# Kernel tuning notes

Hardware: AMD Instinct MI355X
Metric: run time of the kernel (lower is better)

## Reference

```python
import jax, jax.numpy as jnp
import numpy as np

B, F, D = 16384, 256, 128
H = [512, 256]
OUT = 8
VOCAB = 100000


def setup_inputs() -> dict:
    key = jax.random.key(0)
    ks = jax.random.split(key, 16)
    s = lambda k, *sh: jax.random.normal(k, sh, jnp.float32) * 0.05
    return dict(
        features=jax.random.normal(ks[0], (B, F), jnp.float32),
        ent_idx=jax.random.randint(ks[1], (B,), 0, VOCAB),
        target=jax.random.randint(ks[2], (B,), 0, OUT),
        Wf=s(ks[3], F, D), bf=jnp.zeros((D,), jnp.float32),
        Wu=s(ks[4], D, D), bu=jnp.zeros((D,), jnp.float32),
        w_cf=s(ks[5], D), w_fc=s(ks[6], D),
        w_ef=s(ks[7], D), w_fe=s(ks[8], D),
        b_c=jnp.zeros((1,), jnp.float32), b_e=jnp.zeros((1,), jnp.float32),
        head_tab=s(ks[9], VOCAB, D), ent_tab=s(ks[10], VOCAB, D),
        W0=s(ks[11], 2 * D, H[0]), b0=jnp.zeros((H[0],), jnp.float32),
        W1=s(ks[12], H[0], H[1]), b1=jnp.zeros((H[1],), jnp.float32),
        W2=s(ks[13], H[1], OUT), b2=jnp.zeros((OUT,), jnp.float32),
    )


def cross_compress(f, e, w_cf, w_fc, w_ef, w_fe, b_c, b_e):
    # torch code builds c = f (outer) e of shape (B,D,D) then matmuls a (D,1)
    # vector; algebraically (f e^T) w = f * (e . w), so we use the O(B*D) form.
    ew_cf = e @ w_cf  # (B,)
    fw_fc = f @ w_fc
    ew_ef = e @ w_ef
    fw_fe = f @ w_fe
    new_f = f * ew_cf[:, None] + e * fw_fc[:, None] + b_c
    new_e = f * ew_ef[:, None] + e * fw_fe[:, None] + b_e
    return new_f, new_e


def reference(features, ent_idx, target, Wf, bf, Wu, bu, w_cf, w_fc, w_ef,
              w_fe, b_c, b_e, head_tab, ent_tab, W0, b0, W1, b1, W2, b2):
    # 'rec' branch of CompanyOperationEvaluation.forward (eval mode, dropout=id)
    cf = jax.nn.relu(features @ Wf + bf)          # feature_layer
    e = ent_tab[ent_idx]                           # entity_embed lookup
    h = head_tab[ent_idx]                          # head_embed lookup (same ids)
    for _ in range(2):
        cf = jax.nn.relu(cf @ Wu + bu)             # user_low_mlp_layer
        h, e = cross_compress(h, e, w_cf, w_fc, w_ef, w_fe, b_c, b_e)
    high = jnp.concatenate([cf, e], axis=1)        # (B, 2D)
    x = jax.nn.relu(high @ W0 + b0)
    x = jax.nn.relu(x @ W1 + b1)
    x = jax.nn.relu(x @ W2 + b2)                   # pred_last_layer
    prob = jax.nn.softmax(x, axis=1)
    return (prob, target)
```

## Files before the change

kernel.cpp:

```cpp
#include <hip/hip_runtime.h>
#include <hip/hip_bf16.h>


typedef __bf16 bf16x8 __attribute__((ext_vector_type(8)));
typedef float floatx4 __attribute__((ext_vector_type(4)));

__device__ __forceinline__ unsigned short f2bf(float x) {
  unsigned int u = __builtin_bit_cast(unsigned int, x);
  u = (u + 0x7FFFu + ((u >> 16) & 1u)) >> 16;
  return (unsigned short)u;
}
__device__ __forceinline__ float bf2f(unsigned short h) {
  return __builtin_bit_cast(float, (unsigned int)h << 16);
}

__global__ __launch_bounds__(256) void prep_kernel(
    const float* __restrict__ features, const int* __restrict__ ent_idx,
    const float* __restrict__ head_tab, const float* __restrict__ ent_tab,
    const float* __restrict__ Wf, const float* __restrict__ Wu,
    const float* __restrict__ W0, const float* __restrict__ W1,
    const float* __restrict__ W2,
    unsigned short* __restrict__ feat_bf, unsigned short* __restrict__ e_buf,
    unsigned short* __restrict__ h_buf,
    unsigned short* __restrict__ wfT, unsigned short* __restrict__ wuT,
    unsigned short* __restrict__ w0T, unsigned short* __restrict__ w1T,
    unsigned short* __restrict__ w2T) {
  const int bid = blockIdx.x, tid = threadIdx.x;
  if (bid < 2048) {
    size_t base = (size_t)bid * 2048 + (size_t)tid * 8;
    float4 f0 = *(const float4*)(features + base);
    float4 f1 = *(const float4*)(features + base + 4);
    uint4 v;
    v.x = (unsigned)f2bf(f0.x) | ((unsigned)f2bf(f0.y) << 16);
    v.y = (unsigned)f2bf(f0.z) | ((unsigned)f2bf(f0.w) << 16);
    v.z = (unsigned)f2bf(f1.x) | ((unsigned)f2bf(f1.y) << 16);
    v.w = (unsigned)f2bf(f1.z) | ((unsigned)f2bf(f1.w) << 16);
    *(uint4*)(feat_bf + base) = v;
  } else if (bid < 4096) {
    int r = (bid - 2048) * 8 + (tid >> 5);
    int c = (tid & 31) * 4;
    int idx = ent_idx[r];
    float4 ev = *(const float4*)(ent_tab + (size_t)idx * 128 + c);
    float4 hv = *(const float4*)(head_tab + (size_t)idx * 128 + c);
    uint2 eo, ho;
    eo.x = (unsigned)f2bf(ev.x) | ((unsigned)f2bf(ev.y) << 16);
    eo.y = (unsigned)f2bf(ev.z) | ((unsigned)f2bf(ev.w) << 16);
    ho.x = (unsigned)f2bf(hv.x) | ((unsigned)f2bf(hv.y) << 16);
    ho.y = (unsigned)f2bf(hv.z) | ((unsigned)f2bf(hv.w) << 16);
    *(uint2*)(e_buf + (size_t)r * 128 + c) = eo;
    *(uint2*)(h_buf + (size_t)r * 128 + c) = ho;
  } else {
    int g = (bid - 4096) * 256 + tid;
    if (g < 32768) {
      int k = g >> 7, n = g & 127;  wfT[n * 256 + k] = f2bf(Wf[g]);
    } else if (g < 49152) {
      int l = g - 32768; int k = l >> 7, n = l & 127;
      wuT[n * 128 + k] = f2bf(Wu[l]);
    } else if (g < 180224) {
      int l = g - 49152; int k = l >> 9, n = l & 511;
      w0T[n * 256 + k] = f2bf(W0[l]);
    } else if (g < 311296) {
      int l = g - 180224; int k = l >> 8, n = l & 255;
      w1T[n * 512 + k] = f2bf(W1[l]);
    } else {
      int l = g - 311296; int k = l >> 3, n = l & 7;
      w2T[n * 256 + k] = f2bf(W2[l]);
    }
  }
}

__global__ __launch_bounds__(256) void gemm_kernel(
    const unsigned short* __restrict__ A, const unsigned short* __restrict__ BT,
    const float* __restrict__ bias, unsigned short* __restrict__ C,
    int K, int ldc) {
  __shared__ __align__(16) unsigned short a_sh[128 * 72];
  __shared__ __align__(16) unsigned short b_sh[64 * 72];
  const int tid = threadIdx.x;
  const int bn = blockIdx.x, bm = blockIdx.y;
  const int lane = tid & 63;
  const int wave = tid >> 6;
  const int wm = wave & 1, wn = wave >> 1;
  const int m16 = lane & 15, quad = lane >> 4;

  floatx4 acc[4][2];
#pragma unroll
  for (int i = 0; i < 4; ++i)
#pragma unroll
    for (int j = 0; j < 2; ++j) acc[i][j] = (floatx4){0.f, 0.f, 0.f, 0.f};

  for (int k0 = 0; k0 < K; k0 += 64) {
#pragma unroll
    for (int i = 0; i < 4; ++i) {
      int chunk = i * 256 + tid;
      int row = chunk >> 3, seg = chunk & 7;
      *(uint4*)&a_sh[row * 72 + seg * 8] =
          *(const uint4*)(A + (size_t)(bm * 128 + row) * K + k0 + seg * 8);
    }
#pragma unroll
    for (int i = 0; i < 2; ++i) {
      int chunk = i * 256 + tid;
      int row = chunk >> 3, seg = chunk & 7;
      *(uint4*)&b_sh[row * 72 + seg * 8] =
          *(const uint4*)(BT + (size_t)(bn * 64 + row) * K + k0 + seg * 8);
    }
    __syncthreads();
#pragma unroll
    for (int kk = 0; kk < 64; kk += 32) {
      bf16x8 af[4], bfr[2];
#pragma unroll
      for (int mi = 0; mi < 4; ++mi)
        af[mi] = *(const bf16x8*)&a_sh[(wm * 64 + mi * 16 + m16) * 72 + kk + quad * 8];
#pragma unroll
      for (int ni = 0; ni < 2; ++ni)
        bfr[ni] = *(const bf16x8*)&b_sh[(wn * 32 + ni * 16 + m16) * 72 + kk + quad * 8];
#pragma unroll
      for (int mi = 0; mi < 4; ++mi)
#pragma unroll
        for (int ni = 0; ni < 2; ++ni)
          acc[mi][ni] = __builtin_amdgcn_mfma_f32_16x16x32_bf16(
              af[mi], bfr[ni], acc[mi][ni], 0, 0, 0);
    }
    __syncthreads();
  }
#pragma unroll
  for (int mi = 0; mi < 4; ++mi) {
#pragma unroll
    for (int ni = 0; ni < 2; ++ni) {
      int col = bn * 64 + wn * 32 + ni * 16 + m16;
      float bv = bias[col];
#pragma unroll
      for (int r = 0; r < 4; ++r) {
        int row = bm * 128 + wm * 64 + mi * 16 + quad * 4 + r;
        float v = acc[mi][ni][r] + bv;
        v = fmaxf(v, 0.f);
        C[(size_t)row * ldc + col] = f2bf(v);
      }
    }
  }
}

__global__ __launch_bounds__(64) void cross_kernel(
    const unsigned short* __restrict__ h_buf, const unsigned short* __restrict__ e_buf,
    const float* __restrict__ w_cf, const float* __restrict__ w_fc,
    const float* __restrict__ w_ef, const float* __restrict__ w_fe,
    const float* __restrict__ b_c, const float* __restrict__ b_e,
    unsigned short* __restrict__ high) {
  const int lane = threadIdx.x;
  const int rl = lane >> 4, seg = lane & 15;
  const int row = blockIdx.x * 4 + rl;
  const int cb = seg * 8;
  float h[8], e[8], wcf[8], wfc[8], wef[8], wfe[8];
  const unsigned short* hp = h_buf + (size_t)row * 128 + cb;
  const unsigned short* ep = e_buf + (size_t)row * 128 + cb;
#pragma unroll
  for (int j = 0; j < 8; ++j) { h[j] = bf2f(hp[j]); e[j] = bf2f(ep[j]); }
#pragma unroll
  for (int j = 0; j < 8; ++j) {
    wcf[j] = w_cf[cb + j]; wfc[j] = w_fc[cb + j];
    wef[j] = w_ef[cb + j]; wfe[j] = w_fe[cb + j];
  }
  const float bc = b_c[0], be = b_e[0];
#pragma unroll
  for (int it = 0; it < 2; ++it) {
    float d0 = 0, d1 = 0, d2 = 0, d3 = 0;
#pragma unroll
    for (int j = 0; j < 8; ++j) {
      d0 += e[j] * wcf[j];
      d1 += h[j] * wfc[j];
      d2 += e[j] * wef[j];
      d3 += h[j] * wfe[j];
    }
#pragma unroll
    for (int s = 1; s < 16; s <<= 1) {
      d0 += __shfl_xor(d0, s); d1 += __shfl_xor(d1, s);
      d2 += __shfl_xor(d2, s); d3 += __shfl_xor(d3, s);
    }
    float nh[8], ne[8];
#pragma unroll
    for (int j = 0; j < 8; ++j) {
      nh[j] = h[j] * d0 + e[j] * d1 + bc;
      ne[j] = h[j] * d2 + e[j] * d3 + be;
    }
#pragma unroll
    for (int j = 0; j < 8; ++j) { h[j] = nh[j]; e[j] = ne[j]; }
  }
  uint4 v;
  v.x = (unsigned)f2bf(e[0]) | ((unsigned)f2bf(e[1]) << 16);
  v.y = (unsigned)f2bf(e[2]) | ((unsigned)f2bf(e[3]) << 16);
  v.z = (unsigned)f2bf(e[4]) | ((unsigned)f2bf(e[5]) << 16);
  v.w = (unsigned)f2bf(e[6]) | ((unsigned)f2bf(e[7]) << 16);
  *(uint4*)(high + (size_t)row * 256 + 128 + cb) = v;
}

__global__ __launch_bounds__(256) void final_kernel(
    const unsigned short* __restrict__ x1, const unsigned short* __restrict__ w2T,
    const float* __restrict__ b2, const int* __restrict__ target,
    float* __restrict__ out) {
  const int lane = threadIdx.x & 63;
  const int row = blockIdx.x * 4 + (threadIdx.x >> 6);
  float x[4];
  {
    const unsigned short* xp = x1 + (size_t)row * 256 + lane * 4;
#pragma unroll
    for (int j = 0; j < 4; ++j) x[j] = bf2f(xp[j]);
  }
  float p[8];
#pragma unroll
  for (int n = 0; n < 8; ++n) {
    const unsigned short* wp = w2T + n * 256 + lane * 4;
    float s = 0.f;
#pragma unroll
    for (int j = 0; j < 4; ++j) s += x[j] * bf2f(wp[j]);
    p[n] = s;
  }
#pragma unroll
  for (int s = 1; s < 64; s <<= 1) {
#pragma unroll
    for (int n = 0; n < 8; ++n) p[n] += __shfl_xor(p[n], s);
  }
  float mx = -1e30f;
#pragma unroll
  for (int n = 0; n < 8; ++n) {
    p[n] = fmaxf(p[n] + b2[n], 0.f);
    mx = fmaxf(mx, p[n]);
  }
  float sum = 0.f;
#pragma unroll
  for (int n = 0; n < 8; ++n) { p[n] = __expf(p[n] - mx); sum += p[n]; }
  const float inv = 1.f / sum;
  if (lane < 8) out[(size_t)row * 8 + lane] = p[lane] * inv;
  if (lane == 8) out[(size_t)(16384 * 8) + row] = (float)target[row];
}

extern "C" void kernel_launch(void* const* d_in, const int* in_sizes, int n_in,
                              void* d_out, int out_size, void* d_ws, size_t ws_size,
                              hipStream_t stream) {
  const float* features = (const float*)d_in[0];
  const int* ent_idx    = (const int*)d_in[1];
  const int* target     = (const int*)d_in[2];
  const float* Wf  = (const float*)d_in[3];
  const float* bf  = (const float*)d_in[4];
  const float* Wu  = (const float*)d_in[5];
  const float* bu  = (const float*)d_in[6];
  const float* w_cf = (const float*)d_in[7];
  const float* w_fc = (const float*)d_in[8];
  const float* w_ef = (const float*)d_in[9];
  const float* w_fe = (const float*)d_in[10];
  const float* b_c  = (const float*)d_in[11];
  const float* b_e  = (const float*)d_in[12];
  const float* head_tab = (const float*)d_in[13];
  const float* ent_tab  = (const float*)d_in[14];
  const float* W0 = (const float*)d_in[15];
  const float* b0 = (const float*)d_in[16];
  const float* W1 = (const float*)d_in[17];
  const float* b1 = (const float*)d_in[18];
  const float* W2 = (const float*)d_in[19];
  const float* b2 = (const float*)d_in[20];
  float* out = (float*)d_out;

  unsigned short* ws = (unsigned short*)d_ws;
  size_t off = 0;
  auto alloc = [&](size_t n) { unsigned short* p = ws + off; off += n; return p; };
  unsigned short* feat_bf = alloc(16384ull * 256);
  unsigned short* e_buf   = alloc(16384ull * 128);
  unsigned short* h_buf   = alloc(16384ull * 128);
  unsigned short* cf_a    = alloc(16384ull * 128);
  unsigned short* cf_b    = alloc(16384ull * 128);
  unsigned short* high    = alloc(16384ull * 256);
  unsigned short* x0      = alloc(16384ull * 512);
  unsigned short* x1      = alloc(16384ull * 256);
  unsigned short* wfT = alloc(32768);
  unsigned short* wuT = alloc(16384);
  unsigned short* w0T = alloc(131072);
  unsigned short* w1T = alloc(131072);
  unsigned short* w2T = alloc(2048);
  (void)ws_size; (void)in_sizes; (void)n_in; (void)out_size;

  prep_kernel<<<5320, 256, 0, stream>>>(features, ent_idx, head_tab, ent_tab,
      Wf, Wu, W0, W1, W2, feat_bf, e_buf, h_buf, wfT, wuT, w0T, w1T, w2T);
  gemm_kernel<<<dim3(2, 128), 256, 0, stream>>>(feat_bf, wfT, bf, cf_a, 256, 128);
  gemm_kernel<<<dim3(2, 128), 256, 0, stream>>>(cf_a, wuT, bu, cf_b, 128, 128);
  gemm_kernel<<<dim3(2, 128), 256, 0, stream>>>(cf_b, wuT, bu, high, 128, 256);
  cross_kernel<<<4096, 64, 0, stream>>>(h_buf, e_buf, w_cf, w_fc, w_ef, w_fe,
                                        b_c, b_e, high);
  gemm_kernel<<<dim3(8, 128), 256, 0, stream>>>(high, w0T, b0, x0, 256, 512);
  gemm_kernel<<<dim3(4, 128), 256, 0, stream>>>(x0, w1T, b1, x1, 512, 256);
  final_kernel<<<4096, 256, 0, stream>>>(x1, w2T, b2, target, out);
}
```

Before: 219.9 us.

## Fuse cross-compress into gather, chain cf MLP layers, fuse W1 GEMM with head

Folds the cross-compress computation into the embedding-gather prep stage, so h/e no longer round-trip through global memory. The feature cast and the three cf-MLP GEMMs become one kernel that keeps intermediates in LDS. The W1 GEMM is merged with the final W2 projection and softmax. Weight transposes now go through an LDS tile for coalesced writes. Together this cuts eight launches to four and removes several intermediate buffers, but the fused GEMMs read B operands straight from global memory with small 32-row tiles, which may reduce MFMA efficiency.

```diff
diff --git a/kernel.cpp b/kernel.cpp
--- a/kernel.cpp
+++ b/kernel.cpp
@@ -15,56 +15,166 @@
 }
 
 __global__ __launch_bounds__(256) void prep_kernel(
-    const float* __restrict__ features, const int* __restrict__ ent_idx,
-    const float* __restrict__ head_tab, const float* __restrict__ ent_tab,
+    const int* __restrict__ ent_idx, const float* __restrict__ head_tab,
+    const float* __restrict__ ent_tab,
+    const float* __restrict__ w_cf, const float* __restrict__ w_fc,
+    const float* __restrict__ w_ef, const float* __restrict__ w_fe,
+    const float* __restrict__ b_c, const float* __restrict__ b_e,
     const float* __restrict__ Wf, const float* __restrict__ Wu,
     const float* __restrict__ W0, const float* __restrict__ W1,
     const float* __restrict__ W2,
-    unsigned short* __restrict__ feat_bf, unsigned short* __restrict__ e_buf,
-    unsigned short* __restrict__ h_buf,
+    unsigned short* __restrict__ high,
     unsigned short* __restrict__ wfT, unsigned short* __restrict__ wuT,
     unsigned short* __restrict__ w0T, unsigned short* __restrict__ w1T,
     unsigned short* __restrict__ w2T) {
+  __shared__ unsigned short tile[32][34];
   const int bid = blockIdx.x, tid = threadIdx.x;
   if (bid < 2048) {
-    size_t base = (size_t)bid * 2048 + (size_t)tid * 8;
-    float4 f0 = *(const float4*)(features + base);
-    float4 f1 = *(const float4*)(features + base + 4);
-    uint4 v;
-    v.x = (unsigned)f2bf(f0.x) | ((unsigned)f2bf(f0.y) << 16);
-    v.y = (unsigned)f2bf(f0.z) | ((unsigned)f2bf(f0.w) << 16);
-    v.z = (unsigned)f2bf(f1.x) | ((unsigned)f2bf(f1.y) << 16);
-    v.w = (unsigned)f2bf(f1.z) | ((unsigned)f2bf(f1.w) << 16);
-    *(uint4*)(feat_bf + base) = v;
-  } else if (bid < 4096) {
-    int r = (bid - 2048) * 8 + (tid >> 5);
-    int c = (tid & 31) * 4;
-    int idx = ent_idx[r];
+    const int row = bid * 8 + (tid >> 5);
+    const int c = (tid & 31) * 4;
+    const int idx = ent_idx[row];
+    float4 hv = *(const float4*)(head_tab + (size_t)idx * 128 + c);
     float4 ev = *(const float4*)(ent_tab + (size_t)idx * 128 + c);
-    float4 hv = *(const float4*)(head_tab + (size_t)idx * 128 + c);
-    uint2 eo, ho;
-    eo.x = (unsigned)f2bf(ev.x) | ((unsigned)f2bf(ev.y) << 16);
-    eo.y = (unsigned)f2bf(ev.z) | ((unsigned)f2bf(ev.w) << 16);
-    ho.x = (unsigned)f2bf(hv.x) | ((unsigned)f2bf(hv.y) << 16);
-    ho.y = (unsigned)f2bf(hv.z) | ((unsigned)f2bf(hv.w) << 16);
-    *(uint2*)(e_buf + (size_t)r * 128 + c) = eo;
-    *(uint2*)(h_buf + (size_t)r * 128 + c) = ho;
+    float h[4] = {hv.x, hv.y, hv.z, hv.w};
+    float e[4] = {ev.x, ev.y, ev.z, ev.w};
+    float wcf[4], wfc[4], wef[4], wfe[4];
+#pragma unroll
+    for (int j = 0; j < 4; ++j) {
+      wcf[j] = w_cf[c + j]; wfc[j] = w_fc[c + j];
+      wef[j] = w_ef[c + j]; wfe[j] = w_fe[c + j];
+    }
+    const float bc = b_c[0], be = b_e[0];
+#pragma unroll
+    for (int it = 0; it < 2; ++it) {
+      float d0 = 0, d1 = 0, d2 = 0, d3 = 0;
+#pragma unroll
+      for (int j = 0; j < 4; ++j) {
+        d0 += e[j] * wcf[j]; d1 += h[j] * wfc[j];
+        d2 += e[j] * wef[j]; d3 += h[j] * wfe[j];
+      }
+#pragma unroll
+      for (int s = 1; s < 32; s <<= 1) {
+        d0 += __shfl_xor(d0, s); d1 += __shfl_xor(d1, s);
+        d2 += __shfl_xor(d2, s); d3 += __shfl_xor(d3, s);
+      }
+      float nh[4], ne[4];
+#pragma unroll
+      for (int j = 0; j < 4; ++j) {
+        nh[j] = h[j] * d0 + e[j] * d1 + bc;
+        ne[j] = h[j] * d2 + e[j] * d3 + be;
+      }
+#pragma unroll
+      for (int j = 0; j < 4; ++j) { h[j] = nh[j]; e[j] = ne[j]; }
+    }
+    uint2 v;
+    v.x = (unsigned)f2bf(e[0]) | ((unsigned)f2bf(e[1]) << 16);
+    v.y = (unsigned)f2bf(e[2]) | ((unsigned)f2bf(e[3]) << 16);
+    *(uint2*)(high + (size_t)row * 256 + 128 + c) = v;
+  } else if (bid < 2352) {
+    int t = bid - 2048;
+    const float* src; unsigned short* dst; int N, K, kt, nt;
+    if (t < 32)       { src = Wf; dst = wfT; N = 128; K = 256; kt = t >> 2;       nt = t & 3; }
+    else if (t < 48)  { t -= 32;  src = Wu; dst = wuT; N = 128; K = 128; kt = t >> 2; nt = t & 3; }
+    else if (t < 176) { t -= 48;  src = W0; dst = w0T; N = 512; K = 256; kt = t >> 4; nt = t & 15; }
+    else              { t -= 176; src = W1; dst = w1T; N = 256; K = 512; kt = t >> 3; nt = t & 7; }
+    {
+      int r = tid >> 3, cg = (tid & 7) * 4;
+      float4 v = *(const float4*)(src + (size_t)(kt * 32 + r) * N + nt * 32 + cg);
+      tile[r][cg + 0] = f2bf(v.x); tile[r][cg + 1] = f2bf(v.y);
+      tile[r][cg + 2] = f2bf(v.z); tile[r][cg + 3] = f2bf(v.w);
+    }
+    __syncthreads();
+    {
+      int rp = tid >> 3, cg = (tid & 7) * 4;
+      uint2 o;
+      o.x = (unsigned)tile[cg + 0][rp] | ((unsigned)tile[cg + 1][rp] << 16);
+      o.y = (unsigned)tile[cg + 2][rp] | ((unsigned)tile[cg + 3][rp] << 16);
+      *(uint2*)(dst + (size_t)(nt * 32 + rp) * K + kt * 32 + cg) = o;
+    }
   } else {
-    int g = (bid - 4096) * 256 + tid;
-    if (g < 32768) {
-      int k = g >> 7, n = g & 127;  wfT[n * 256 + k] = f2bf(Wf[g]);
-    } else if (g < 49152) {
-      int l = g - 32768; int k = l >> 7, n = l & 127;
-      wuT[n * 128 + k] = f2bf(Wu[l]);
-    } else if (g < 180224) {
-      int l = g - 49152; int k = l >> 9, n = l & 511;
-      w0T[n * 256 + k] = f2bf(W0[l]);
-    } else if (g < 311296) {
-      int l = g - 180224; int k = l >> 8, n = l & 255;
-      w1T[n * 512 + k] = f2bf(W1[l]);
-    } else {
-      int l = g - 311296; int k = l >> 3, n = l & 7;
-      w2T[n * 256 + k] = f2bf(W2[l]);
+#pragma unroll
+    for (int i = 0; i < 8; ++i) {
+      int g = tid * 8 + i, k = g >> 3, n = g & 7;
+      w2T[n * 256 + k] = f2bf(W2[g]);
+    }
+  }
+}
+
+template <int K, int LDA>
+__device__ __forceinline__ void mfma_layer(const unsigned short* A_sh,
+                                           const unsigned short* __restrict__ BT,
+                                           int rw, int nc, floatx4 acc[4]) {
+  const int lane = threadIdx.x & 63;
+  const int m16 = lane & 15, quad = lane >> 4;
+#pragma unroll
+  for (int nt = 0; nt < 4; ++nt) acc[nt] = (floatx4){0.f, 0.f, 0.f, 0.f};
+#pragma unroll
+  for (int kk = 0; kk < K; kk += 32) {
+    bf16x8 a = *(const bf16x8*)&A_sh[(rw + m16) * LDA + kk + quad * 8];
+#pragma unroll
+    for (int nt = 0; nt < 4; ++nt) {
+      bf16x8 b = *(const bf16x8*)(BT + (size_t)(nc + nt * 16 + m16) * K + kk + quad * 8);
+      acc[nt] = __builtin_amdgcn_mfma_f32_16x16x32_bf16(a, b, acc[nt], 0, 0, 0);
+    }
+  }
+}
+
+__device__ __forceinline__ void epi_lds(const floatx4 acc[4],
+                                        const float* __restrict__ bias, int rw,
+                                        int nc, unsigned short* buf, int ldb) {
+  const int lane = threadIdx.x & 63;
+  const int m16 = lane & 15, quad = lane >> 4;
+#pragma unroll
+  for (int nt = 0; nt < 4; ++nt) {
+    int col = nc + nt * 16 + m16;
+    float bv = bias[col];
+#pragma unroll
+    for (int r = 0; r < 4; ++r)
+      buf[(rw + quad * 4 + r) * ldb + col] = f2bf(fmaxf(acc[nt][r] + bv, 0.f));
+  }
+}
+
+__global__ __launch_bounds__(256) void cf_chain_kernel(
+    const float* __restrict__ features, const unsigned short* __restrict__ wfT,
+    const unsigned short* __restrict__ wuT, const float* __restrict__ bf_,
+    const float* __restrict__ bu, unsigned short* __restrict__ high) {
+  __shared__ __align__(16) unsigned short feat_sh[32 * 264];
+  __shared__ __align__(16) unsigned short buf0[32 * 136];
+  __shared__ __align__(16) unsigned short buf1[32 * 136];
+  const int tid = threadIdx.x;
+  const int r0 = blockIdx.x * 32;
+  {
+    int row = tid >> 3, c0 = (tid & 7) * 4;
+#pragma unroll
+    for (int i = 0; i < 8; ++i) {
+      int c = c0 + i * 32;
+      float4 v = *(const float4*)(features + (size_t)(r0 + row) * 256 + c);
+      uint2 o;
+      o.x = (unsigned)f2bf(v.x) | ((unsigned)f2bf(v.y) << 16);
+      o.y = (unsigned)f2bf(v.z) | ((unsigned)f2bf(v.w) << 16);
+      *(uint2*)&feat_sh[row * 264 + c] = o;
+    }
+  }
+  __syncthreads();
+  const int wave = tid >> 6;
+  const int rw = (wave >> 1) * 16, nc = (wave & 1) * 64;
+  floatx4 acc[4];
+  mfma_layer<256, 264>(feat_sh, wfT, rw, nc, acc);
+  epi_lds(acc, bf_, rw, nc, buf0, 136);
+  __syncthreads();
+  mfma_layer<128, 136>(buf0, wuT, rw, nc, acc);
+  epi_lds(acc, bu, rw, nc, buf1, 136);
+  __syncthreads();
+  mfma_layer<128, 136>(buf1, wuT, rw, nc, acc);
+  const int lane = tid & 63, m16 = lane & 15, quad = lane >> 4;
+#pragma unroll
+  for (int nt = 0; nt < 4; ++nt) {
+    int col = nc + nt * 16 + m16;
+    float bv = bu[col];
+#pragma unroll
+    for (int r = 0; r < 4; ++r) {
+      int row = r0 + rw + quad * 4 + r;
+      high[(size_t)row * 256 + col] = f2bf(fmaxf(acc[nt][r] + bv, 0.f));
     }
   }
 }
@@ -131,105 +241,96 @@
 #pragma unroll
       for (int r = 0; r < 4; ++r) {
         int row = bm * 128 + wm * 64 + mi * 16 + quad * 4 + r;
-        float v = acc[mi][ni][r] + bv;
-        v = fmaxf(v, 0.f);
+        float v = fmaxf(acc[mi][ni][r] + bv, 0.f);
         C[(size_t)row * ldc + col] = f2bf(v);
       }
     }
   }
 }
 
-__global__ __launch_bounds__(64) void cross_kernel(
-    const unsigned short* __restrict__ h_buf, const unsigned short* __restrict__ e_buf,
-    const float* __restrict__ w_cf, const float* __restrict__ w_fc,
-    const float* __restrict__ w_ef, const float* __restrict__ w_fe,
-    const float* __restrict__ b_c, const float* __restrict__ b_e,
-    unsigned short* __restrict__ high) {
-  const int lane = threadIdx.x;
-  const int rl = lane >> 4, seg = lane & 15;
-  const int row = blockIdx.x * 4 + rl;
-  const int cb = seg * 8;
-  float h[8], e[8], wcf[8], wfc[8], wef[8], wfe[8];
-  const unsigned short* hp = h_buf + (size_t)row * 128 + cb;
-  const unsigned short* ep = e_buf + (size_t)row * 128 + cb;
-#pragma unroll
-  for (int j = 0; j < 8; ++j) { h[j] = bf2f(hp[j]); e[j] = bf2f(ep[j]); }
-#pragma unroll
-  for (int j = 0; j < 8; ++j) {
-    wcf[j] = w_cf[cb + j]; wfc[j] = w_fc[cb + j];
-    wef[j] = w_ef[cb + j]; wfe[j] = w_fe[cb + j];
-  }
-  const float bc = b_c[0], be = b_e[0];
-#pragma unroll
-  for (int it = 0; it < 2; ++it) {
-    float d0 = 0, d1 = 0, d2 = 0, d3 = 0;
-#pragma unroll
-    for (int j = 0; j < 8; ++j) {
-      d0 += e[j] * wcf[j];
-      d1 += h[j] * wfc[j];
-      d2 += e[j] * wef[j];
-      d3 += h[j] * wfe[j];
-    }
-#pragma unroll
-    for (int s = 1; s < 16; s <<= 1) {
-      d0 += __shfl_xor(d0, s); d1 += __shfl_xor(d1, s);
-      d2 += __shfl_xor(d2, s); d3 += __shfl_xor(d3, s);
-    }
-    float nh[8], ne[8];
-#pragma unroll
-    for (int j = 0; j < 8; ++j) {
-      nh[j] = h[j] * d0 + e[j] * d1 + bc;
-      ne[j] = h[j] * d2 + e[j] * d3 + be;
-    }
-#pragma unroll
-    for (int j = 0; j < 8; ++j) { h[j] = nh[j]; e[j] = ne[j]; }
-  }
-  uint4 v;
-  v.x = (unsigned)f2bf(e[0]) | ((unsigned)f2bf(e[1]) << 16);
-  v.y = (unsigned)f2bf(e[2]) | ((unsigned)f2bf(e[3]) << 16);
-  v.z = (unsigned)f2bf(e[4]) | ((unsigned)f2bf(e[5]) << 16);
-  v.w = (unsigned)f2bf(e[6]) | ((unsigned)f2bf(e[7]) << 16);
-  *(uint4*)(high + (size_t)row * 256 + 128 + cb) = v;
-}
-
-__global__ __launch_bounds__(256) void final_kernel(
-    const unsigned short* __restrict__ x1, const unsigned short* __restrict__ w2T,
+__global__ __launch_bounds__(256) void gemm_w1_final_kernel(
+    const unsigned short* __restrict__ x0, const unsigned short* __restrict__ w1T,
+    const float* __restrict__ b1, const unsigned short* __restrict__ w2T,
     const float* __restrict__ b2, const int* __restrict__ target,
     float* __restrict__ out) {
-  const int lane = threadIdx.x & 63;
-  const int row = blockIdx.x * 4 + (threadIdx.x >> 6);
-  float x[4];
+  __shared__ __align__(16) unsigned short a_sh[32 * 72];
+  __shared__ __align__(16) unsigned short x1_sh[32 * 264];
+  __shared__ __align__(16) unsigned short w2_sh[2048];
+  const int tid = threadIdx.x;
+  const int r0 = blockIdx.x * 32;
+  *(uint4*)&w2_sh[tid * 8] = *(const uint4*)(w2T + tid * 8);
+  const int lane = tid & 63, wave = tid >> 6;
+  const int m16 = lane & 15, quad = lane >> 4;
+  const int rw = (wave >> 1) * 16, nc = (wave & 1) * 128;
+  floatx4 acc[8];
+#pragma unroll
+  for (int nt = 0; nt < 8; ++nt) acc[nt] = (floatx4){0.f, 0.f, 0.f, 0.f};
+  for (int k0 = 0; k0 < 512; k0 += 64) {
+    __syncthreads();
+    {
+      int row = tid >> 3, seg = tid & 7;
+      *(uint4*)&a_sh[row * 72 + seg * 8] =
+          *(const uint4*)(x0 + (size_t)(r0 + row) * 512 + k0 + seg * 8);
+    }
+    __syncthreads();
+#pragma unroll
+    for (int kk = 0; kk < 64; kk += 32) {
+      bf16x8 a = *(const bf16x8*)&a_sh[(rw + m16) * 72 + kk + quad * 8];
+#pragma unroll
+      for (int nt = 0; nt < 8; ++nt) {
+        bf16x8 b = *(const bf16x8*)(w1T + (size_t)(nc + nt * 16 + m16) * 512 +
+                                    k0 + kk + quad * 8);
+        acc[nt] = __builtin_amdgcn_mfma_f32_16x16x32_bf16(a, b, acc[nt], 0, 0, 0);
+      }
+    }
+  }
+#pragma unroll
+  for (int nt = 0; nt < 8; ++nt) {
+    int col = nc + nt * 16 + m16;
+    float bv = b1[col];
+#pragma unroll
+    for (int r = 0; r < 4; ++r)
+      x1_sh[(rw + quad * 4 + r) * 264 + col] = f2bf(fmaxf(acc[nt][r] + bv, 0.f));
+  }
+  __syncthreads();
   {
-    const unsigned short* xp = x1 + (size_t)row * 256 + lane * 4;
-#pragma unroll
-    for (int j = 0; j < 4; ++j) x[j] = bf2f(xp[j]);
-  }
-  float p[8];
-#pragma unroll
-  for (int n = 0; n < 8; ++n) {
-    const unsigned short* wp = w2T + n * 256 + lane * 4;
-    float s = 0.f;
-#pragma unroll
-    for (int j = 0; j < 4; ++j) s += x[j] * bf2f(wp[j]);
-    p[n] = s;
-  }
-#pragma unroll
-  for (int s = 1; s < 64; s <<= 1) {
-#pragma unroll
-    for (int n = 0; n < 8; ++n) p[n] += __shfl_xor(p[n], s);
-  }
-  float mx = -1e30f;
-#pragma unroll
-  for (int n = 0; n < 8; ++n) {
-    p[n] = fmaxf(p[n] + b2[n], 0.f);
-    mx = fmaxf(mx, p[n]);
-  }
-  float sum = 0.f;
-#pragma unroll
-  for (int n = 0; n < 8; ++n) { p[n] = __expf(p[n] - mx); sum += p[n]; }
-  const float inv = 1.f / sum;
-  if (lane < 8) out[(size_t)row * 8 + lane] = p[lane] * inv;
-  if (lane == 8) out[(size_t)(16384 * 8) + row] = (float)target[row];
+    int row = tid >> 3, q = tid & 7;
+    float p[8];
+#pragma unroll
+    for (int n = 0; n < 8; ++n) p[n] = 0.f;
+#pragma unroll
+    for (int jb = 0; jb < 4; ++jb) {
+      bf16x8 xv = *(const bf16x8*)&x1_sh[row * 264 + q * 32 + jb * 8];
+#pragma unroll
+      for (int n = 0; n < 8; ++n) {
+        bf16x8 wv = *(const bf16x8*)&w2_sh[n * 256 + q * 32 + jb * 8];
+#pragma unroll
+        for (int j = 0; j < 8; ++j) p[n] += (float)xv[j] * (float)wv[j];
+      }
+    }
+#pragma unroll
+    for (int s = 1; s < 8; s <<= 1)
+#pragma unroll
+      for (int n = 0; n < 8; ++n) p[n] += __shfl_xor(p[n], s);
+    if (q == 0) {
+      float mx = -1e30f;
+#pragma unroll
+      for (int n = 0; n < 8; ++n) {
+        p[n] = fmaxf(p[n] + b2[n], 0.f);
+        mx = fmaxf(mx, p[n]);
+      }
+      float sum = 0.f;
+#pragma unroll
+      for (int n = 0; n < 8; ++n) { p[n] = __expf(p[n] - mx); sum += p[n]; }
+      const float inv = 1.f / sum;
+      const int gr = r0 + row;
+      float4 o0 = {p[0] * inv, p[1] * inv, p[2] * inv, p[3] * inv};
+      float4 o1 = {p[4] * inv, p[5] * inv, p[6] * inv, p[7] * inv};
+      *(float4*)(out + (size_t)gr * 8) = o0;
+      *(float4*)(out + (size_t)gr * 8 + 4) = o1;
+      out[16384 * 8 + gr] = (float)target[gr];
+    }
+  }
 }
 
 extern "C" void kernel_launch(void* const* d_in, const int* in_sizes, int n_in,
@@ -239,7 +340,7 @@
   const int* ent_idx    = (const int*)d_in[1];
   const int* target     = (const int*)d_in[2];
   const float* Wf  = (const float*)d_in[3];
-  const float* bf  = (const float*)d_in[4];
+  const float* bf_ = (const float*)d_in[4];
   const float* Wu  = (const float*)d_in[5];
   const float* bu  = (const float*)d_in[6];
   const float* w_cf = (const float*)d_in[7];
@@ -261,29 +362,19 @@
   unsigned short* ws = (unsigned short*)d_ws;
   size_t off = 0;
   auto alloc = [&](size_t n) { unsigned short* p = ws + off; off += n; return p; };
-  unsigned short* feat_bf = alloc(16384ull * 256);
-  unsigned short* e_buf   = alloc(16384ull * 128);
-  unsigned short* h_buf   = alloc(16384ull * 128);
-  unsigned short* cf_a    = alloc(16384ull * 128);
-  unsigned short* cf_b    = alloc(16384ull * 128);
-  unsigned short* high    = alloc(16384ull * 256);
-  unsigned short* x0      = alloc(16384ull * 512);
-  unsigned short* x1      = alloc(16384ull * 256);
-  unsigned short* wfT = alloc(32768);
-  unsigned short* wuT = alloc(16384);
-  unsigned short* w0T = alloc(131072);
-  unsigned short* w1T = alloc(131072);
-  unsigned short* w2T = alloc(2048);
+  unsigned short* high = alloc(16384ull * 256);
+  unsigned short* x0   = alloc(16384ull * 512);
+  unsigned short* wfT  = alloc(32768);
+  unsigned short* wuT  = alloc(16384);
+  unsigned short* w0T  = alloc(131072);
+  unsigned short* w1T  = alloc(131072);
+  unsigned short* w2T  = alloc(2048);
   (void)ws_size; (void)in_sizes; (void)n_in; (void)out_size;
 
-  prep_kernel<<<5320, 256, 0, stream>>>(features, ent_idx, head_tab, ent_tab,
-      Wf, Wu, W0, W1, W2, feat_bf, e_buf, h_buf, wfT, wuT, w0T, w1T, w2T);
-  gemm_kernel<<<dim3(2, 128), 256, 0, stream>>>(feat_bf, wfT, bf, cf_a, 256, 128);
-  gemm_kernel<<<dim3(2, 128), 256, 0, stream>>>(cf_a, wuT, bu, cf_b, 128, 128);
-  gemm_kernel<<<dim3(2, 128), 256, 0, stream>>>(cf_b, wuT, bu, high, 128, 256);
-  cross_kernel<<<4096, 64, 0, stream>>>(h_buf, e_buf, w_cf, w_fc, w_ef, w_fe,
-                                        b_c, b_e, high);
+  prep_kernel<<<2353, 256, 0, stream>>>(ent_idx, head_tab, ent_tab,
+      w_cf, w_fc, w_ef, w_fe, b_c, b_e, Wf, Wu, W0, W1, W2,
+      high, wfT, wuT, w0T, w1T, w2T);
+  cf_chain_kernel<<<512, 256, 0, stream>>>(features, wfT, wuT, bf_, bu, high);
   gemm_kernel<<<dim3(8, 128), 256, 0, stream>>>(high, w0T, b0, x0, 256, 512);
-  gemm_kernel<<<dim3(4, 128), 256, 0, stream>>>(x0, w1T, b1, x1, 512, 256);
-  final_kernel<<<4096, 256, 0, stream>>>(x1, w2T, b2, target, out);
-}
+  gemm_w1_final_kernel<<<512, 256, 0, stream>>>(x0, w1T, b1, w2T, b2, target, out);
+}
```

New measurement: 230.8 us. +5.0%, slower.
